# Kernel optimization log

Measured on AMD Instinct MI355X. Metric: run time of the kernel, lower is better.

Reference implementation:

```python
import jax, jax.numpy as jnp
import numpy as np

HEADS = 8  # matches init_kwargs

def setup_inputs() -> dict:
    key = jax.random.key(0)
    ks = jax.random.split(key, 13)
    N, L, E = 4, 256, 256
    H = HEADS
    D = E // H
    s = 0.05
    inp = {
        'values': jax.random.normal(ks[0], (N, L, E), jnp.float32) * s,
        'keys': jax.random.normal(ks[1], (N, L, E), jnp.float32) * s,
        'query': jax.random.normal(ks[2], (N, L, E), jnp.float32) * s,
        'mask': jax.random.randint(ks[3], (N, 1, L, L, 1), 0, 2, dtype=jnp.int32),
        'relation': jax.random.normal(ks[4], (N, L, L, E), jnp.float32) * s,
        # per-head projection weights (nn.Linear, bias=False): y = x @ W.T
        'Wv': jax.random.normal(ks[5], (D, D), jnp.float32) * s,
        'Wk': jax.random.normal(ks[6], (D, D), jnp.float32) * s,
        'Wq': jax.random.normal(ks[7], (D, D), jnp.float32) * s,
        'Wr': jax.random.normal(ks[8], (D, D), jnp.float32) * s,
        'Wfuse': jax.random.normal(ks[9], (D, 2 * D), jnp.float32) * s,
        'bfuse': jax.random.normal(ks[10], (D,), jnp.float32) * s,
        'Wout': jax.random.normal(ks[11], (E, E), jnp.float32) * s,
        'bout': jax.random.normal(ks[12], (E,), jnp.float32) * s,
    }
    return inp


def reference(values, keys, query, mask, relation, Wv, Wk, Wq, Wr, Wfuse, bfuse, Wout, bout):
    N, Q, E = query.shape
    K = keys.shape[1]
    H = HEADS
    D = E // H
    # split heads
    v = values.reshape(N, K, H, D)
    k = keys.reshape(N, K, H, D)
    q = query.reshape(N, Q, H, D)
    r = relation.reshape(N, Q, K, H, D)
    # per-head linear projections (x @ W.T)
    v = jnp.einsum('nlhd,od->nlho', v, Wv)
    k = jnp.einsum('nlhd,od->nlho', k, Wk)
    q = jnp.einsum('nqhd,od->nqho', q, Wq)
    r = jnp.einsum('nqkhd,od->nqkho', r, Wr)
    r = jnp.transpose(r, (0, 3, 1, 2, 4))  # (N,H,Q,K,D)
    # outer-product scores, no reduction over d: (N,H,Q,K,D)
    energy = jnp.einsum('nqhd,nkhd->nhqkd', q, k)
    energy = jnp.concatenate([energy, r], axis=-1)  # (N,H,Q,K,2D)
    energy = jnp.einsum('nhqkf,df->nhqkd', energy, Wfuse) + bfuse  # fc_fuse
    energy = energy.sum(axis=-1)  # (N,H,Q,K)  (keepdim squeezed; same math)
    # masked_fill(mask == 1, -1e20)
    energy = jnp.where(mask[..., 0] == 1, jnp.float32(-1e20), energy)
    attn = jax.nn.softmax(energy / jnp.sqrt(jnp.float32(E)), axis=3)
    out = jnp.einsum('nhqk,nkhd->nqhd', attn, v).reshape(N, Q, E)
    out = out @ Wout.T + bout  # fc_out
    return out
```

## Files before the change

kernel.cpp:

```cpp
#include <hip/hip_runtime.h>
#include <hip/hip_bf16.h>

#define LSEQ 256
#define EDIM 256
#define HNUM 8
#define DDIM 32
#define NBAT 4

#define OFF_QS   0
#define OFF_KP   (NBAT*LSEQ*EDIM)
#define OFF_VP   (2*NBAT*LSEQ*EDIM)
#define OFF_WOT  (3*NBAT*LSEQ*EDIM)
#define OFF_WA   (3*NBAT*LSEQ*EDIM + EDIM*EDIM)
#define OFF_WR   (OFF_WA + 32)
#define OFF_BS   (OFF_WR + 32)
#define OFF_EN   852096
#define WS_NEED_FLOATS (OFF_EN + NBAT*LSEQ*LSEQ*HNUM)

__global__ __launch_bounds__(256)
void prep_all(const float* __restrict__ query, const float* __restrict__ keys,
              const float* __restrict__ values,
              const float* __restrict__ Wq, const float* __restrict__ Wk,
              const float* __restrict__ Wv,
              const float* __restrict__ Wfuse, const float* __restrict__ bfuse,
              const float* __restrict__ Wr, const float* __restrict__ Wout,
              float* __restrict__ ws) {
    int t = threadIdx.x;
    int b = blockIdx.x;
    if (b < 256) {
        __shared__ float xq[4][EDIM], xk[4][EDIM], xv[4][EDIM];
        __shared__ float wqT[DDIM][DDIM + 1], wkT[DDIM][DDIM + 1], wvT[DDIM][DDIM + 1];
        __shared__ float swA[DDIM];
        int row0 = b * 4;
#pragma unroll
        for (int rr = 0; rr < 4; ++rr) {
            xq[rr][t] = query[(row0 + rr) * EDIM + t];
            xk[rr][t] = keys[(row0 + rr) * EDIM + t];
            xv[rr][t] = values[(row0 + rr) * EDIM + t];
        }
        for (int c = t; c < DDIM * DDIM; c += 256) {
            int o = c / DDIM, d = c % DDIM;
            wqT[d][o] = Wq[c];
            wkT[d][o] = Wk[c];
            wvT[d][o] = Wv[c];
        }
        if (t < DDIM) {
            float s = 0.f;
            for (int d = 0; d < DDIM; ++d) s += Wfuse[d * 2 * DDIM + t];
            swA[t] = s;
        }
        __syncthreads();
        int o = t & (DDIM - 1), h = t >> 5;
#pragma unroll
        for (int rr = 0; rr < 4; ++rr) {
            float aq = 0.f, ak = 0.f, av = 0.f;
            for (int d = 0; d < DDIM; ++d) {
                float q_ = xq[rr][h * DDIM + d], k_ = xk[rr][h * DDIM + d], v_ = xv[rr][h * DDIM + d];
                aq += q_ * wqT[d][o];
                ak += k_ * wkT[d][o];
                av += v_ * wvT[d][o];
            }
            ws[OFF_QS + (row0 + rr) * EDIM + t] = aq * swA[o];
            ws[OFF_KP + (row0 + rr) * EDIM + t] = ak;
            ws[OFF_VP + (row0 + rr) * EDIM + t] = av;
        }
    } else if (b < 272) {
        __shared__ float tile[64][65];
        int bb = b - 256;
        int br = bb >> 2, bc = bb & 3;
        int R0 = br * 64, C0 = bc * 64;
        for (int idx = t; idx < 4096; idx += 256) {
            int lr = idx >> 6, lc = idx & 63;
            tile[lr][lc] = Wout[(R0 + lr) * EDIM + C0 + lc];
        }
        __syncthreads();
        for (int idx = t; idx < 4096; idx += 256) {
            int lr = idx >> 6, lc = idx & 63;
            ws[OFF_WOT + (C0 + lr) * EDIM + R0 + lc] = tile[lc][lr];
        }
    } else {
        __shared__ float sWB[DDIM];
        if (t >= DDIM && t < 2 * DDIM) {
            float s = 0.f;
            for (int d = 0; d < DDIM; ++d) s += Wfuse[d * 2 * DDIM + t];
            sWB[t - DDIM] = s;
        }
        if (t == 0) {
            float bs = 0.f;
            for (int d = 0; d < DDIM; ++d) bs += bfuse[d];
            ws[OFF_BS] = bs;
        }
        __syncthreads();
        if (t < DDIM) {
            float s = 0.f;
            for (int o = 0; o < DDIM; ++o) s += sWB[o] * Wr[o * DDIM + t];
            ws[OFF_WR + t] = s;
        }
    }
}

__global__ __launch_bounds__(256, 6)
void energy_kernel(const float* __restrict__ relation, const int* __restrict__ mask,
                   const float* __restrict__ ws, float* __restrict__ en) {
    int t = threadIdx.x;
    int lane = t & 63, wid = t >> 6;
    int wgl = blockIdx.x * 4 + wid;
    int nq = wgl >> 4;
    int k0 = (wgl & 15) * 16;
    int n = nq >> 8;
    int h = lane >> 3;

    const float4* qs4 = reinterpret_cast<const float4*>(ws + OFF_QS);
    const float4* wr4 = reinterpret_cast<const float4*>(ws + OFF_WR);
    float4 qv = qs4[(size_t)nq * 64 + lane];
    float4 wv = wr4[lane & 7];
    float bsum = ws[OFF_BS];

    const float4* rel4 = reinterpret_cast<const float4*>(relation)
                         + (size_t)nq * LSEQ * (EDIM / 4);
    const float4* kp4  = reinterpret_cast<const float4*>(ws + OFF_KP)
                         + (size_t)n * LSEQ * (EDIM / 4);
    const int* mrow = mask + nq * LSEQ;
    float* erow = en + (size_t)nq * (LSEQ * HNUM);

    int mks[16];
#pragma unroll
    for (int j = 0; j < 16; ++j) mks[j] = mrow[k0 + j];

#pragma unroll
    for (int j = 0; j < 16; ++j) {
        int k = k0 + j;
        if (mks[j]) {
            if ((lane & 7) == 0) erow[k * HNUM + h] = -6.25e18f;
        } else {
            float4 rv = rel4[(size_t)k * (EDIM / 4) + lane];
            float4 kv = kp4[(size_t)k * (EDIM / 4) + lane];
            float p = rv.x * wv.x + rv.y * wv.y + rv.z * wv.z + rv.w * wv.w
                    + qv.x * kv.x + qv.y * kv.y + qv.z * kv.z + qv.w * kv.w;
            p += __shfl_xor(p, 1);
            p += __shfl_xor(p, 2);
            p += __shfl_xor(p, 4);
            if ((lane & 7) == 0) erow[k * HNUM + h] = (p + bsum) * 0.0625f;
        }
    }
}

__global__ __launch_bounds__(1024)
void attn_tail4(const float* __restrict__ en, const float* __restrict__ ws,
                const float* __restrict__ bout, float* __restrict__ out) {
    __shared__ float att[4][HNUM][LSEQ + 1];
    __shared__ float part[16][4][EDIM];
    __shared__ float accsm[4][EDIM];

    int t = threadIdx.x;
    int nq0 = blockIdx.x * 4;
    int n = nq0 >> 8;
    int lane = t & 63, wid = t >> 6;
    int e0 = 4 * lane;
    int hh = lane >> 3;

    const float4* en4 = reinterpret_cast<const float4*>(en + (size_t)nq0 * 2048);
#pragma unroll
    for (int j = t; j < 2048; j += 1024) {
        float4 v = en4[j];
        int qq = j >> 9;
        int jj = j & 511;
        int k = jj >> 1, hb = (jj & 1) * 4;
        att[qq][hb + 0][k] = v.x;
        att[qq][hb + 1][k] = v.y;
        att[qq][hb + 2][k] = v.z;
        att[qq][hb + 3][k] = v.w;
    }
    __syncthreads();

    {
        int row = t >> 5, sub = t & 31;
        int qq = row >> 3, h = row & 7;
        float m = -3.4e38f;
        for (int jj = 0; jj < 8; ++jj) m = fmaxf(m, att[qq][h][sub + jj * 32]);
        for (int off = 1; off < 32; off <<= 1) m = fmaxf(m, __shfl_xor(m, off));
        float ex[8];
        float ssum = 0.f;
        for (int jj = 0; jj < 8; ++jj) {
            float e_ = __expf(att[qq][h][sub + jj * 32] - m);
            ex[jj] = e_;
            ssum += e_;
        }
        for (int off = 1; off < 32; off <<= 1) ssum += __shfl_xor(ssum, off);
        float inv = 1.0f / ssum;
        for (int jj = 0; jj < 8; ++jj) att[qq][h][sub + jj * 32] = ex[jj] * inv;
    }
    __syncthreads();

    const float4* vp4 = reinterpret_cast<const float4*>(ws + OFF_VP)
                        + (size_t)n * LSEQ * (EDIM / 4);
    {
        float4 a0 = {0,0,0,0}, a1 = {0,0,0,0}, a2 = {0,0,0,0}, a3 = {0,0,0,0};
#pragma unroll 4
        for (int kk = 0; kk < 16; ++kk) {
            int k = wid * 16 + kk;
            float4 vv = vp4[(size_t)k * (EDIM / 4) + lane];
            float s0 = att[0][hh][k], s1 = att[1][hh][k];
            float s2 = att[2][hh][k], s3 = att[3][hh][k];
            a0.x += s0 * vv.x; a0.y += s0 * vv.y; a0.z += s0 * vv.z; a0.w += s0 * vv.w;
            a1.x += s1 * vv.x; a1.y += s1 * vv.y; a1.z += s1 * vv.z; a1.w += s1 * vv.w;
            a2.x += s2 * vv.x; a2.y += s2 * vv.y; a2.z += s2 * vv.z; a2.w += s2 * vv.w;
            a3.x += s3 * vv.x; a3.y += s3 * vv.y; a3.z += s3 * vv.z; a3.w += s3 * vv.w;
        }
        *reinterpret_cast<float4*>(&part[wid][0][e0]) = a0;
        *reinterpret_cast<float4*>(&part[wid][1][e0]) = a1;
        *reinterpret_cast<float4*>(&part[wid][2][e0]) = a2;
        *reinterpret_cast<float4*>(&part[wid][3][e0]) = a3;
    }
    __syncthreads();
    {
        int qq = t >> 8, e = t & 255;
        float s = 0.f;
#pragma unroll
        for (int w = 0; w < 16; ++w) s += part[w][qq][e];
        accsm[qq][e] = s;
    }
    __syncthreads();

    const float4* wo4 = reinterpret_cast<const float4*>(ws + OFF_WOT);
    {
        float4 o0 = {0,0,0,0}, o1 = {0,0,0,0}, o2 = {0,0,0,0}, o3 = {0,0,0,0};
#pragma unroll 4
        for (int ee = 0; ee < 16; ++ee) {
            int ep = wid * 16 + ee;
            float a0 = accsm[0][ep], a1 = accsm[1][ep];
            float a2 = accsm[2][ep], a3 = accsm[3][ep];
            float4 w = wo4[(size_t)ep * (EDIM / 4) + lane];
            o0.x += a0 * w.x; o0.y += a0 * w.y; o0.z += a0 * w.z; o0.w += a0 * w.w;
            o1.x += a1 * w.x; o1.y += a1 * w.y; o1.z += a1 * w.z; o1.w += a1 * w.w;
            o2.x += a2 * w.x; o2.y += a2 * w.y; o2.z += a2 * w.z; o2.w += a2 * w.w;
            o3.x += a3 * w.x; o3.y += a3 * w.y; o3.z += a3 * w.z; o3.w += a3 * w.w;
        }
        *reinterpret_cast<float4*>(&part[wid][0][e0]) = o0;
        *reinterpret_cast<float4*>(&part[wid][1][e0]) = o1;
        *reinterpret_cast<float4*>(&part[wid][2][e0]) = o2;
        *reinterpret_cast<float4*>(&part[wid][3][e0]) = o3;
    }
    __syncthreads();
    {
        int qq = t >> 8, e = t & 255;
        float s = bout[e];
#pragma unroll
        for (int w = 0; w < 16; ++w) s += part[w][qq][e];
        out[(size_t)(nq0 + qq) * EDIM + e] = s;
    }
}

__global__ __launch_bounds__(256)
void attn_main(const float* __restrict__ relation, const int* __restrict__ mask,
               const float* __restrict__ ws, const float* __restrict__ bout,
               float* __restrict__ out) {
    __shared__ float qs[EDIM];
    __shared__ float wrf[EDIM];
    __shared__ int   mrow[LSEQ];
    __shared__ float energy[HNUM][LSEQ + 1];
    __shared__ float part[4][EDIM];
    __shared__ float accsm[EDIM];
    __shared__ float sb;

    int t = threadIdx.x;
    int bid = blockIdx.x;
    int n = bid >> 8, qi = bid & 255;
    int lane = t & 63, wid = t >> 6;

    qs[t]  = ws[OFF_QS + (n * LSEQ + qi) * EDIM + t];
    wrf[t] = ws[OFF_WR + (t & (DDIM - 1))];
    mrow[t] = mask[(n * LSEQ + qi) * LSEQ + t];
    if (t == 0) sb = ws[OFF_BS];
    __syncthreads();
    float bsum = sb;

    const float4* rel4 = reinterpret_cast<const float4*>(relation)
                         + (size_t)(n * LSEQ + qi) * LSEQ * (EDIM / 4);
    const float4* kp4  = reinterpret_cast<const float4*>(ws + OFF_KP)
                         + (size_t)n * LSEQ * (EDIM / 4);
    int e0 = 4 * lane;
    int hh = lane >> 3;
    float4 qv = *reinterpret_cast<const float4*>(&qs[e0]);
    float4 wv = *reinterpret_cast<const float4*>(&wrf[e0]);
    for (int it = 0; it < 64; ++it) {
        int k = it * 4 + wid;
        float4 rv = rel4[(size_t)k * (EDIM / 4) + lane];
        float4 kv = kp4[(size_t)k * (EDIM / 4) + lane];
        float p = rv.x * wv.x + rv.y * wv.y + rv.z * wv.z + rv.w * wv.w
                + qv.x * kv.x + qv.y * kv.y + qv.z * kv.z + qv.w * kv.w;
        p += __shfl_xor(p, 1);
        p += __shfl_xor(p, 2);
        p += __shfl_xor(p, 4);
        if ((lane & 7) == 0) {
            float val = mrow[k] ? -1e20f : (p + bsum);
            energy[hh][k] = val * 0.0625f;
        }
    }
    __syncthreads();

    {
        int h = t >> 5, sub = t & 31;
        float m = -3.4e38f;
        for (int jj = 0; jj < 8; ++jj) m = fmaxf(m, energy[h][sub + jj * 32]);
        for (int off = 1; off < 32; off <<= 1) m = fmaxf(m, __shfl_xor(m, off));
        float ex[8];
        float ssum = 0.f;
        for (int jj = 0; jj < 8; ++jj) {
            float e_ = __expf(energy[h][sub + jj * 32] - m);
            ex[jj] = e_;
            ssum += e_;
        }
        for (int off = 1; off < 32; off <<= 1) ssum += __shfl_xor(ssum, off);
        float inv = 1.0f / ssum;
        for (int jj = 0; jj < 8; ++jj) energy[h][sub + jj * 32] = ex[jj] * inv;
    }
    __syncthreads();

    const float4* vp4 = reinterpret_cast<const float4*>(ws + OFF_VP)
                        + (size_t)n * LSEQ * (EDIM / 4);
    {
        float4 a4 = {0.f, 0.f, 0.f, 0.f};
        for (int kk = 0; kk < 64; ++kk) {
            int k = wid * 64 + kk;
            float4 vv = vp4[(size_t)k * (EDIM / 4) + lane];
            float a = energy[hh][k];
            a4.x += a * vv.x; a4.y += a * vv.y; a4.z += a * vv.z; a4.w += a * vv.w;
        }
        *reinterpret_cast<float4*>(&part[wid][e0]) = a4;
    }
    __syncthreads();
    accsm[t] = part[0][t] + part[1][t] + part[2][t] + part[3][t];
    __syncthreads();

    const float4* wo4 = reinterpret_cast<const float4*>(ws + OFF_WOT);
    {
        float4 o4 = {0.f, 0.f, 0.f, 0.f};
        for (int ee = 0; ee < 64; ++ee) {
            int ep = wid * 64 + ee;
            float a = accsm[ep];
            float4 w = wo4[(size_t)ep * (EDIM / 4) + lane];
            o4.x += a * w.x; o4.y += a * w.y; o4.z += a * w.z; o4.w += a * w.w;
        }
        *reinterpret_cast<float4*>(&part[wid][e0]) = o4;
    }
    __syncthreads();
    out[(n * LSEQ + qi) * EDIM + t] =
        part[0][t] + part[1][t] + part[2][t] + part[3][t] + bout[t];
}

extern "C" void kernel_launch(void* const* d_in, const int* in_sizes, int n_in,
                              void* d_out, int out_size, void* d_ws, size_t ws_size,
                              hipStream_t stream) {
    const float* values   = (const float*)d_in[0];
    const float* keys     = (const float*)d_in[1];
    const float* query    = (const float*)d_in[2];
    const int*   mask     = (const int*)d_in[3];
    const float* relation = (const float*)d_in[4];
    const float* Wv    = (const float*)d_in[5];
    const float* Wk    = (const float*)d_in[6];
    const float* Wq    = (const float*)d_in[7];
    const float* Wr    = (const float*)d_in[8];
    const float* Wfuse = (const float*)d_in[9];
    const float* bfuse = (const float*)d_in[10];
    const float* Wout  = (const float*)d_in[11];
    const float* bout  = (const float*)d_in[12];
    float* ws  = (float*)d_ws;
    float* out = (float*)d_out;

    prep_all<<<273, 256, 0, stream>>>(query, keys, values,
                                      Wq, Wk, Wv, Wfuse, bfuse,
                                      Wr, Wout, ws);

    if (ws_size >= (size_t)WS_NEED_FLOATS * sizeof(float)) {
        float* en = ws + OFF_EN;
        energy_kernel<<<4096, 256, 0, stream>>>(relation, mask, ws, en);
        attn_tail4<<<NBAT * LSEQ / 4, 1024, 0, stream>>>(en, ws, bout, out);
    } else {
        attn_main<<<NBAT * LSEQ, 256, 0, stream>>>(relation, mask, ws, bout, out);
    }
}
```

Baseline: 47.65 us.

## Store energies head-major with float4 writes, vectorize prep loads and mask reads

The energy buffer is switched from a [k][h] layout to a [h][k] layout. This lets each head lane write four consecutive key energies as one float4 instead of 16 scattered scalar stores, and the tail kernel's shared-memory unpack is updated to match. The prep kernel now handles 8 rows per block with float4 global loads and half as many blocks. The mask is read as int4, and the energy kernel's occupancy hint drops from 6 to 4 blocks per CU, which may reduce latency hiding on the main relation stream.

```diff
diff --git a/kernel.cpp b/kernel.cpp
--- a/kernel.cpp
+++ b/kernel.cpp
@@ -27,16 +27,20 @@
               float* __restrict__ ws) {
     int t = threadIdx.x;
     int b = blockIdx.x;
-    if (b < 256) {
-        __shared__ float xq[4][EDIM], xk[4][EDIM], xv[4][EDIM];
+    if (b < 128) {
+        __shared__ float xq[8][EDIM], xk[8][EDIM], xv[8][EDIM];
         __shared__ float wqT[DDIM][DDIM + 1], wkT[DDIM][DDIM + 1], wvT[DDIM][DDIM + 1];
         __shared__ float swA[DDIM];
-        int row0 = b * 4;
-#pragma unroll
-        for (int rr = 0; rr < 4; ++rr) {
-            xq[rr][t] = query[(row0 + rr) * EDIM + t];
-            xk[rr][t] = keys[(row0 + rr) * EDIM + t];
-            xv[rr][t] = values[(row0 + rr) * EDIM + t];
+        int row0 = b * 8;
+        const float4* q4 = reinterpret_cast<const float4*>(query + (size_t)row0 * EDIM);
+        const float4* k4 = reinterpret_cast<const float4*>(keys + (size_t)row0 * EDIM);
+        const float4* v4 = reinterpret_cast<const float4*>(values + (size_t)row0 * EDIM);
+#pragma unroll
+        for (int idx = t; idx < 512; idx += 256) {
+            int rr = idx >> 6, c4 = (idx & 63) * 4;
+            *reinterpret_cast<float4*>(&xq[rr][c4]) = q4[idx];
+            *reinterpret_cast<float4*>(&xk[rr][c4]) = k4[idx];
+            *reinterpret_cast<float4*>(&xv[rr][c4]) = v4[idx];
         }
         for (int c = t; c < DDIM * DDIM; c += 256) {
             int o = c / DDIM, d = c % DDIM;
@@ -52,7 +56,7 @@
         __syncthreads();
         int o = t & (DDIM - 1), h = t >> 5;
 #pragma unroll
-        for (int rr = 0; rr < 4; ++rr) {
+        for (int rr = 0; rr < 8; ++rr) {
             float aq = 0.f, ak = 0.f, av = 0.f;
             for (int d = 0; d < DDIM; ++d) {
                 float q_ = xq[rr][h * DDIM + d], k_ = xk[rr][h * DDIM + d], v_ = xv[rr][h * DDIM + d];
@@ -60,13 +64,13 @@
                 ak += k_ * wkT[d][o];
                 av += v_ * wvT[d][o];
             }
-            ws[OFF_QS + (row0 + rr) * EDIM + t] = aq * swA[o];
-            ws[OFF_KP + (row0 + rr) * EDIM + t] = ak;
-            ws[OFF_VP + (row0 + rr) * EDIM + t] = av;
-        }
-    } else if (b < 272) {
+            ws[OFF_QS + (size_t)(row0 + rr) * EDIM + t] = aq * swA[o];
+            ws[OFF_KP + (size_t)(row0 + rr) * EDIM + t] = ak;
+            ws[OFF_VP + (size_t)(row0 + rr) * EDIM + t] = av;
+        }
+    } else if (b < 144) {
         __shared__ float tile[64][65];
-        int bb = b - 256;
+        int bb = b - 128;
         int br = bb >> 2, bc = bb & 3;
         int R0 = br * 64, C0 = bc * 64;
         for (int idx = t; idx < 4096; idx += 256) {
@@ -99,7 +103,7 @@
     }
 }
 
-__global__ __launch_bounds__(256, 6)
+__global__ __launch_bounds__(256, 4)
 void energy_kernel(const float* __restrict__ relation, const int* __restrict__ mask,
                    const float* __restrict__ ws, float* __restrict__ en) {
     int t = threadIdx.x;
@@ -120,28 +124,43 @@
                          + (size_t)nq * LSEQ * (EDIM / 4);
     const float4* kp4  = reinterpret_cast<const float4*>(ws + OFF_KP)
                          + (size_t)n * LSEQ * (EDIM / 4);
-    const int* mrow = mask + nq * LSEQ;
-    float* erow = en + (size_t)nq * (LSEQ * HNUM);
-
+
+    const int4* m4 = reinterpret_cast<const int4*>(mask + (size_t)nq * LSEQ + k0);
     int mks[16];
 #pragma unroll
-    for (int j = 0; j < 16; ++j) mks[j] = mrow[k0 + j];
-
-#pragma unroll
-    for (int j = 0; j < 16; ++j) {
-        int k = k0 + j;
-        if (mks[j]) {
-            if ((lane & 7) == 0) erow[k * HNUM + h] = -6.25e18f;
-        } else {
-            float4 rv = rel4[(size_t)k * (EDIM / 4) + lane];
-            float4 kv = kp4[(size_t)k * (EDIM / 4) + lane];
-            float p = rv.x * wv.x + rv.y * wv.y + rv.z * wv.z + rv.w * wv.w
-                    + qv.x * kv.x + qv.y * kv.y + qv.z * kv.z + qv.w * kv.w;
-            p += __shfl_xor(p, 1);
-            p += __shfl_xor(p, 2);
-            p += __shfl_xor(p, 4);
-            if ((lane & 7) == 0) erow[k * HNUM + h] = (p + bsum) * 0.0625f;
-        }
+    for (int g = 0; g < 4; ++g) {
+        int4 mm = m4[g];
+        mks[g * 4 + 0] = mm.x; mks[g * 4 + 1] = mm.y;
+        mks[g * 4 + 2] = mm.z; mks[g * 4 + 3] = mm.w;
+    }
+
+    float* erow = en + (size_t)nq * (LSEQ * HNUM) + h * LSEQ;
+
+#pragma unroll
+    for (int g = 0; g < 4; ++g) {
+        float4 acc;
+        float* ap = &acc.x;
+#pragma unroll
+        for (int j4 = 0; j4 < 4; ++j4) {
+            int j = g * 4 + j4;
+            int k = k0 + j;
+            float val;
+            if (mks[j]) {
+                val = -6.25e18f;
+            } else {
+                float4 rv = rel4[(size_t)k * (EDIM / 4) + lane];
+                float4 kv = kp4[(size_t)k * (EDIM / 4) + lane];
+                float p = rv.x * wv.x + rv.y * wv.y + rv.z * wv.z + rv.w * wv.w
+                        + qv.x * kv.x + qv.y * kv.y + qv.z * kv.z + qv.w * kv.w;
+                p += __shfl_xor(p, 1);
+                p += __shfl_xor(p, 2);
+                p += __shfl_xor(p, 4);
+                val = (p + bsum) * 0.0625f;
+            }
+            ap[j4] = val;
+        }
+        if ((lane & 7) == 0)
+            *reinterpret_cast<float4*>(&erow[k0 + g * 4]) = acc;
     }
 }
 
@@ -164,12 +183,12 @@
     for (int j = t; j < 2048; j += 1024) {
         float4 v = en4[j];
         int qq = j >> 9;
-        int jj = j & 511;
-        int k = jj >> 1, hb = (jj & 1) * 4;
-        att[qq][hb + 0][k] = v.x;
-        att[qq][hb + 1][k] = v.y;
-        att[qq][hb + 2][k] = v.z;
-        att[qq][hb + 3][k] = v.w;
+        int r = j & 511;
+        int h = r >> 6, k4 = (r & 63) * 4;
+        att[qq][h][k4 + 0] = v.x;
+        att[qq][h][k4 + 1] = v.y;
+        att[qq][h][k4 + 2] = v.z;
+        att[qq][h][k4 + 3] = v.w;
     }
     __syncthreads();
 
@@ -368,7 +387,7 @@
     float* ws  = (float*)d_ws;
     float* out = (float*)d_out;
 
-    prep_all<<<273, 256, 0, stream>>>(query, keys, values,
+    prep_all<<<145, 256, 0, stream>>>(query, keys, values,
                                       Wq, Wk, Wv, Wfuse, bfuse,
                                       Wr, Wout, ws);
 
```

Measured after the change: 55.50 us. 1.16x slower.
